# Kernel optimization log

Measured on AMD Instinct MI355X. Metric: run time of the kernel, lower is better.

## Reference

```python
import jax, jax.numpy as jnp
import numpy as np

B, T, A, F, K, DQ, DV = 64, 1024, 128, 1024, 31, 1024, 512  # filters F == T required by source math


def setup_inputs() -> dict:
    key = jax.random.key(0)
    ks = jax.random.split(key, 8)
    s = 0.05
    return {
        "query": jax.random.normal(ks[0], (B, 1, DQ), jnp.float32),
        "value": jax.random.normal(ks[1], (B, T, DV), jnp.float32),
        "attention_weights_cat": jax.random.uniform(ks[2], (B, T, 2), jnp.float32),
        "Wq": jax.random.normal(ks[3], (DQ, A), jnp.float32) * s,
        "Wm": jax.random.normal(ks[4], (DV, A), jnp.float32) * s,
        "Wv": jax.random.normal(ks[5], (A, 1), jnp.float32) * s,
        "Wconv": jax.random.normal(ks[6], (K, 2, F), jnp.float32) * s,
        "Wloc": jax.random.normal(ks[7], (T, A), jnp.float32) * s,
    }


def reference(query, value, attention_weights_cat, Wq, Wm, Wv, Wconv, Wloc):
    # query_layer: Dense(tanh, no bias): [B,1,DQ] -> [B,1,A]
    q = jnp.tanh(jnp.einsum('bld,da->bla', query, Wq))
    # memory_layer: Dense(tanh, no bias): [B,T,DV] -> [B,T,A]
    v = jnp.tanh(jnp.einsum('btd,da->bta', value, Wm))
    # location conv (SAME, no bias): [B,T,2] -> [B,T,F]
    loc = jax.lax.conv_general_dilated(
        attention_weights_cat, Wconv, window_strides=(1,), padding='SAME',
        dimension_numbers=('NWC', 'WIO', 'NWC'))
    # source transposes [0,2,1] then Dense(T->A, tanh): [B,F,T] -> [B,F,A]
    loc = jnp.tanh(jnp.einsum('bft,ta->bfa', jnp.transpose(loc, (0, 2, 1)), Wloc))
    # additive score (F == T so broadcast add is element-aligned): [B,T,1]
    score = jnp.einsum('bta,ao->bto', jnp.tanh(q + v + loc), Wv)
    alignment = jax.nn.softmax(score, axis=1)                # softmax over time
    context = jnp.sum(alignment * v, axis=1)                  # [B,A]
    return context, jnp.transpose(alignment, (0, 2, 1))       # [B,1,T]
```

## Files before the change

kernel.cpp:

```cpp
#include <hip/hip_runtime.h>
#include <hip/hip_bf16.h>

#define BB 64
#define TT 1024
#define AA 128
#define FF 1024
#define DQ 1024
#define DV 512

typedef __bf16 bf16x8_t __attribute__((ext_vector_type(8)));
typedef __bf16 bf16x4_t __attribute__((ext_vector_type(4)));
typedef float f32x4_t __attribute__((ext_vector_type(4)));
typedef _Float16 f16x4_t __attribute__((ext_vector_type(4)));

__device__ __forceinline__ float ftanh(float x) {
    float e = __expf(2.0f * x);
    return 1.0f - 2.0f / (e + 1.0f);
}

__device__ __forceinline__ __bf16 bhi(float x) { return (__bf16)x; }
__device__ __forceinline__ __bf16 blo(float x) {
    __bf16 h = (__bf16)x;
    return (__bf16)(x - (float)h);
}

__global__ __launch_bounds__(256) void k_prep(
    const float* __restrict__ Wm, const float* __restrict__ Wconv,
    const float* __restrict__ Wloc, const float* __restrict__ query,
    const float* __restrict__ Wq,
    __bf16* __restrict__ pwmhi, __bf16* __restrict__ pwmlo,
    __bf16* __restrict__ wcthi, __bf16* __restrict__ wctlo,
    __bf16* __restrict__ pwlhi, __bf16* __restrict__ pwllo,
    float* __restrict__ q_ws) {
    __shared__ float ls[128 * 65];
    int bx = blockIdx.x, tid = threadIdx.x;
    if (bx < 16) {
        int s = bx, d0 = s * 32;
        for (int i = tid; i < 4096; i += 256) {
            int dd = i >> 7, a = i & 127;
            ls[a * 33 + dd] = Wm[(d0 + dd) * AA + a];
        }
        __syncthreads();
#pragma unroll
        for (int u = 0; u < 2; u++) {
            int pos = tid * 2 + u;
            int l15 = pos & 15, lq = (pos >> 4) & 3, g = pos >> 6;
            bf16x8_t h8, l8;
#pragma unroll
            for (int j = 0; j < 8; j++) {
                float x = ls[(g * 16 + l15) * 33 + lq * 8 + j];
                h8[j] = bhi(x);
                l8[j] = blo(x);
            }
            size_t off = (size_t)(s * 512 + pos) * 8;
            *(bf16x8_t*)(pwmhi + off) = h8;
            *(bf16x8_t*)(pwmlo + off) = l8;
        }
    } else if (bx < 24) {
        int f0 = (bx - 16) * 128;
        for (int i = tid; i < 8192; i += 256) {
            int kc = i >> 7, f = i & 127;
            ls[f * 65 + kc] = (kc < 62) ? Wconv[kc * FF + f0 + f] : 0.f;
        }
        __syncthreads();
        int f = tid >> 1, half = tid & 1;
#pragma unroll
        for (int g = 0; g < 4; g++) {
            bf16x8_t h8, l8;
#pragma unroll
            for (int j = 0; j < 8; j++) {
                float x = ls[f * 65 + half * 32 + g * 8 + j];
                h8[j] = bhi(x);
                l8[j] = blo(x);
            }
            size_t off = (size_t)(f0 + f) * 64 + half * 32 + g * 8;
            *(bf16x8_t*)(wcthi + off) = h8;
            *(bf16x8_t*)(wctlo + off) = l8;
        }
    } else if (bx < 56) {
        int s2 = bx - 24, t0 = s2 * 32;
        for (int i = tid; i < 4096; i += 256) {
            int tt = i >> 7, a = i & 127;
            ls[a * 33 + tt] = Wloc[(t0 + tt) * AA + a];
        }
        __syncthreads();
#pragma unroll
        for (int u = 0; u < 2; u++) {
            int pos = tid * 2 + u;
            int l15 = pos & 15, lq = (pos >> 4) & 3, g = pos >> 6;
            bf16x8_t h8, l8;
#pragma unroll
            for (int j = 0; j < 8; j++) {
                float x = ls[(g * 16 + l15) * 33 + lq * 8 + j];
                h8[j] = bhi(x);
                l8[j] = blo(x);
            }
            size_t off = (size_t)(s2 * 512 + pos) * 8;
            *(bf16x8_t*)(pwlhi + off) = h8;
            *(bf16x8_t*)(pwllo + off) = l8;
        }
    } else {
        int b = bx - 56;
        int a = tid & 127, half = tid >> 7;
        const float* qrow = query + b * DQ + half * 512;
        float a0 = 0.f, a1 = 0.f, a2 = 0.f, a3 = 0.f;
        for (int d = 0; d < 512; d += 4) {
            float4 qv = *(const float4*)(qrow + d);
            int dg = (half * 512 + d) * AA + a;
            a0 += qv.x * Wq[dg];
            a1 += qv.y * Wq[dg + AA];
            a2 += qv.z * Wq[dg + 2 * AA];
            a3 += qv.w * Wq[dg + 3 * AA];
        }
        ls[tid] = a0 + a1 + a2 + a3;
        __syncthreads();
        if (half == 0) q_ws[b * AA + a] = ftanh(ls[a] + ls[a + 128]);
    }
}

__global__ __launch_bounds__(256) void k_zq(
    const float* __restrict__ xcat,
    const __bf16* __restrict__ pwlhi, const __bf16* __restrict__ pwllo,
    __bf16* __restrict__ zthi, __bf16* __restrict__ ztlo) {
    int b = blockIdx.x, tid = threadIdx.x;
    __shared__ float xs0[1056], xs1[1056];
    __shared__ float zs[64 * 132];
    for (int i = tid; i < 1056; i += 256) {
        int t = i - 16;
        float2 xv = (t >= 0 && t < TT) ? *(const float2*)(xcat + (size_t)(b * TT + t) * 2)
                                       : make_float2(0.f, 0.f);
        xs0[i] = xv.x;
        xs1[i] = xv.y;
    }
    __syncthreads();
    int lane = tid & 63, wid = tid >> 6;
    int wm = wid >> 1, wn = wid & 1;
    int l15 = lane & 15, lq = lane >> 4;

    f32x4_t zacc[2][4];
#pragma unroll
    for (int mi = 0; mi < 2; mi++)
#pragma unroll
        for (int ni = 0; ni < 4; ni++) zacc[mi][ni] = (f32x4_t){0.f, 0.f, 0.f, 0.f};

    for (int s = 0; s < 32; s++) {
        int t0 = s * 32;
        bf16x8_t bh[4], bl[4];
#pragma unroll
        for (int ni = 0; ni < 4; ni++) {
            size_t poff = (size_t)((s * 8 + wn * 4 + ni) * 64 + lane) * 8;
            bh[ni] = *(const bf16x8_t*)(pwlhi + poff);
            bl[ni] = *(const bf16x8_t*)(pwllo + poff);
        }
        bf16x8_t ah[2], al[2];
#pragma unroll
        for (int mi = 0; mi < 2; mi++) {
            int kc = wm * 32 + mi * 16 + l15;
            const float* xsc = (kc & 1) ? xs1 : xs0;
            int base = t0 + lq * 8 + (kc >> 1) + 1;
#pragma unroll
            for (int j = 0; j < 8; j++) {
                float x = xsc[base + j];
                ah[mi][j] = bhi(x);
                al[mi][j] = blo(x);
            }
        }
#pragma unroll
        for (int ni = 0; ni < 4; ni++)
#pragma unroll
            for (int mi = 0; mi < 2; mi++) {
                zacc[mi][ni] = __builtin_amdgcn_mfma_f32_16x16x32_bf16(ah[mi], bh[ni], zacc[mi][ni], 0, 0, 0);
                zacc[mi][ni] = __builtin_amdgcn_mfma_f32_16x16x32_bf16(al[mi], bh[ni], zacc[mi][ni], 0, 0, 0);
                zacc[mi][ni] = __builtin_amdgcn_mfma_f32_16x16x32_bf16(ah[mi], bl[ni], zacc[mi][ni], 0, 0, 0);
            }
    }
#pragma unroll
    for (int mi = 0; mi < 2; mi++)
#pragma unroll
        for (int ni = 0; ni < 4; ni++)
#pragma unroll
            for (int r = 0; r < 4; r++)
                zs[(wm * 32 + mi * 16 + lq * 4 + r) * 132 + wn * 64 + ni * 16 + l15] = zacc[mi][ni][r];
    __syncthreads();
    int a = tid >> 1, half = tid & 1;
#pragma unroll
    for (int g = 0; g < 4; g++) {
        bf16x8_t h8, l8;
#pragma unroll
        for (int j = 0; j < 8; j++) {
            float x = zs[(half * 32 + g * 8 + j) * 132 + a];
            h8[j] = bhi(x);
            l8[j] = blo(x);
        }
        size_t off = ((size_t)b * AA + a) * 64 + half * 32 + g * 8;
        *(bf16x8_t*)(zthi + off) = h8;
        *(bf16x8_t*)(ztlo + off) = l8;
    }
}

__global__ __launch_bounds__(256) void k_main(
    const float* __restrict__ value,
    const __bf16* __restrict__ pwmhi, const __bf16* __restrict__ pwmlo,
    const __bf16* __restrict__ wcthi, const __bf16* __restrict__ wctlo,
    const __bf16* __restrict__ zthi, const __bf16* __restrict__ ztlo,
    const float* __restrict__ q_ws, const float* __restrict__ Wv,
    _Float16* __restrict__ v_ws, float* __restrict__ score) {
    int b = blockIdx.x >> 3;
    int trow0 = (blockIdx.x & 7) << 7;
    int tid = threadIdx.x;
    int lane = tid & 63, wid = tid >> 6;
    int wm = wid >> 1, wn = wid & 1;
    int l15 = lane & 15, lq = lane >> 4;

    __shared__ __bf16 as_hi[128 * 40];
    __shared__ __bf16 as_lo[128 * 40];
    __shared__ float sc_red[256];

    f32x4_t acc[4][4];
#pragma unroll
    for (int mi = 0; mi < 4; mi++)
#pragma unroll
        for (int ni = 0; ni < 4; ni++) acc[mi][ni] = (f32x4_t){0.f, 0.f, 0.f, 0.f};

    const float* vbase = value + (size_t)(b * TT + trow0) * DV;
    int t0r = tid >> 3, c4 = tid & 7;
    float4 cur[4];
#pragma unroll
    for (int l = 0; l < 4; l++)
        cur[l] = *(const float4*)(vbase + (size_t)(t0r + 32 * l) * DV + c4 * 4);

    for (int it = 0; it < 16; ++it) {
        int d0 = it * 32;
        bf16x8_t bh[4], bl[4];
#pragma unroll
        for (int ni = 0; ni < 4; ni++) {
            size_t poff = (size_t)((it * 8 + wn * 4 + ni) * 64 + lane) * 8;
            bh[ni] = *(const bf16x8_t*)(pwmhi + poff);
            bl[ni] = *(const bf16x8_t*)(pwmlo + poff);
        }
        __syncthreads();
#pragma unroll
        for (int l = 0; l < 4; l++) {
            int t = t0r + 32 * l;
            float4 v4 = cur[l];
            bf16x4_t hv, lv;
            hv[0] = bhi(v4.x); lv[0] = blo(v4.x);
            hv[1] = bhi(v4.y); lv[1] = blo(v4.y);
            hv[2] = bhi(v4.z); lv[2] = blo(v4.z);
            hv[3] = bhi(v4.w); lv[3] = blo(v4.w);
            *(bf16x4_t*)(as_hi + t * 40 + c4 * 4) = hv;
            *(bf16x4_t*)(as_lo + t * 40 + c4 * 4) = lv;
        }
        __syncthreads();
        if (it < 15) {
#pragma unroll
            for (int l = 0; l < 4; l++)
                cur[l] = *(const float4*)(vbase + (size_t)(t0r + 32 * l) * DV + d0 + 32 + c4 * 4);
        }
        bf16x8_t ah[4], al[4];
#pragma unroll
        for (int mi = 0; mi < 4; mi++) {
            int off2 = (wm * 64 + mi * 16 + l15) * 40 + lq * 8;
            ah[mi] = *(const bf16x8_t*)(as_hi + off2);
            al[mi] = *(const bf16x8_t*)(as_lo + off2);
        }
#pragma unroll
        for (int mi = 0; mi < 4; mi++)
#pragma unroll
            for (int ni = 0; ni < 4; ni++) {
                acc[mi][ni] = __builtin_amdgcn_mfma_f32_16x16x32_bf16(ah[mi], bh[ni], acc[mi][ni], 0, 0, 0);
                acc[mi][ni] = __builtin_amdgcn_mfma_f32_16x16x32_bf16(al[mi], bh[ni], acc[mi][ni], 0, 0, 0);
                acc[mi][ni] = __builtin_amdgcn_mfma_f32_16x16x32_bf16(ah[mi], bl[ni], acc[mi][ni], 0, 0, 0);
            }
    }

    f32x4_t lacc[4][4];
#pragma unroll
    for (int mi = 0; mi < 4; mi++)
#pragma unroll
        for (int ni = 0; ni < 4; ni++) lacc[mi][ni] = (f32x4_t){0.f, 0.f, 0.f, 0.f};
#pragma unroll
    for (int kc0 = 0; kc0 < 64; kc0 += 32) {
        bf16x8_t a2h[4], a2l[4], b2h[4], b2l[4];
#pragma unroll
        for (int mi = 0; mi < 4; mi++) {
            int f = trow0 + wm * 64 + mi * 16 + l15;
            a2h[mi] = *(const bf16x8_t*)(wcthi + (size_t)f * 64 + kc0 + lq * 8);
            a2l[mi] = *(const bf16x8_t*)(wctlo + (size_t)f * 64 + kc0 + lq * 8);
        }
#pragma unroll
        for (int ni = 0; ni < 4; ni++) {
            int a = wn * 64 + ni * 16 + l15;
            size_t off = ((size_t)b * AA + a) * 64 + kc0 + lq * 8;
            b2h[ni] = *(const bf16x8_t*)(zthi + off);
            b2l[ni] = *(const bf16x8_t*)(ztlo + off);
        }
#pragma unroll
        for (int mi = 0; mi < 4; mi++)
#pragma unroll
            for (int ni = 0; ni < 4; ni++) {
                lacc[mi][ni] = __builtin_amdgcn_mfma_f32_16x16x32_bf16(a2h[mi], b2h[ni], lacc[mi][ni], 0, 0, 0);
                lacc[mi][ni] = __builtin_amdgcn_mfma_f32_16x16x32_bf16(a2l[mi], b2h[ni], lacc[mi][ni], 0, 0, 0);
                lacc[mi][ni] = __builtin_amdgcn_mfma_f32_16x16x32_bf16(a2h[mi], b2l[ni], lacc[mi][ni], 0, 0, 0);
            }
    }

    float qv[4], wv[4];
#pragma unroll
    for (int ni = 0; ni < 4; ni++) {
        int a = wn * 64 + ni * 16 + l15;
        qv[ni] = q_ws[b * AA + a];
        wv[ni] = Wv[a];
    }
#pragma unroll
    for (int mi = 0; mi < 4; mi++) {
#pragma unroll
        for (int r = 0; r < 4; r++) {
            int tl = wm * 64 + mi * 16 + lq * 4 + r;
            int t = trow0 + tl;
            float s = 0.f;
#pragma unroll
            for (int ni = 0; ni < 4; ni++) {
                float v = ftanh(acc[mi][ni][r]);
                float loc = ftanh(lacc[mi][ni][r]);
                int a = wn * 64 + ni * 16 + l15;
                v_ws[(size_t)(b * TT + t) * AA + a] = (_Float16)v;
                s += ftanh(qv[ni] + v + loc) * wv[ni];
            }
            s += __shfl_xor(s, 1, 64);
            s += __shfl_xor(s, 2, 64);
            s += __shfl_xor(s, 4, 64);
            s += __shfl_xor(s, 8, 64);
            if (l15 == 0) sc_red[wn * 128 + tl] = s;
        }
    }
    __syncthreads();
    if (tid < 128) score[b * TT + trow0 + tid] = sc_red[tid] + sc_red[128 + tid];
}

__global__ void k_softmax(const float* __restrict__ score, float* __restrict__ out_align) {
    int b = blockIdx.x, tid = threadIdx.x;
    __shared__ float red[4];
    float s[4];
#pragma unroll
    for (int i = 0; i < 4; i++) s[i] = score[b * TT + tid + i * 256];
    float m = fmaxf(fmaxf(s[0], s[1]), fmaxf(s[2], s[3]));
    for (int off = 32; off; off >>= 1) m = fmaxf(m, __shfl_xor(m, off, 64));
    int wid = tid >> 6;
    if ((tid & 63) == 0) red[wid] = m;
    __syncthreads();
    float M = fmaxf(fmaxf(red[0], red[1]), fmaxf(red[2], red[3]));
    __syncthreads();
    float e[4];
    float sum = 0.f;
#pragma unroll
    for (int i = 0; i < 4; i++) { e[i] = __expf(s[i] - M); sum += e[i]; }
    for (int off = 32; off; off >>= 1) sum += __shfl_xor(sum, off, 64);
    if ((tid & 63) == 0) red[wid] = sum;
    __syncthreads();
    float inv = 1.0f / (red[0] + red[1] + red[2] + red[3]);
#pragma unroll
    for (int i = 0; i < 4; i++) out_align[b * TT + tid + i * 256] = e[i] * inv;
}

__global__ void k_context(const float* __restrict__ align, const _Float16* __restrict__ v_ws,
                          float* __restrict__ out_ctx) {
    int b = blockIdx.y, t0 = blockIdx.x * 64, tid = threadIdx.x;
    int a0 = (tid & 31) * 4, tl = tid >> 5;
    __shared__ float sh[8 * 132];
    f32x4_t acc = (f32x4_t){0.f, 0.f, 0.f, 0.f};
    for (int tt = tl; tt < 64; tt += 8) {
        float w = align[b * TT + t0 + tt];
        f16x4_t vv = *(const f16x4_t*)(v_ws + (size_t)(b * TT + t0 + tt) * AA + a0);
        acc[0] += w * (float)vv[0];
        acc[1] += w * (float)vv[1];
        acc[2] += w * (float)vv[2];
        acc[3] += w * (float)vv[3];
    }
    *(f32x4_t*)&sh[tl * 132 + a0] = acc;
    __syncthreads();
    if (tid < 128) {
        float s = 0.f;
#pragma unroll
        for (int j = 0; j < 8; j++) s += sh[j * 132 + tid];
        atomicAdd(out_ctx + b * AA + tid, s);
    }
}

extern "C" void kernel_launch(void* const* d_in, const int* in_sizes, int n_in,
                              void* d_out, int out_size, void* d_ws, size_t ws_size,
                              hipStream_t stream) {
    const float* query = (const float*)d_in[0];
    const float* value = (const float*)d_in[1];
    const float* xcat  = (const float*)d_in[2];
    const float* Wq    = (const float*)d_in[3];
    const float* Wm    = (const float*)d_in[4];
    const float* Wv    = (const float*)d_in[5];
    const float* Wconv = (const float*)d_in[6];
    const float* Wloc  = (const float*)d_in[7];
    float* out = (float*)d_out;

    float* ws = (float*)d_ws;
    float* q_ws  = ws;
    float* sc_ws = q_ws + 8192;
    _Float16* v_ws = (_Float16*)(sc_ws + 65536);
    __bf16* pwmhi = (__bf16*)(sc_ws + 65536 + 4194304);
    __bf16* pwmlo = pwmhi + 65536;
    __bf16* wcthi = pwmlo + 65536;
    __bf16* wctlo = wcthi + 65536;
    __bf16* pwlhi = wctlo + 65536;
    __bf16* pwllo = pwlhi + 131072;
    __bf16* zthi  = pwllo + 131072;
    __bf16* ztlo  = zthi + 524288;

    (void)hipMemsetAsync(out, 0, (size_t)8192 * 4, stream);

    k_prep<<<120, 256, 0, stream>>>(Wm, Wconv, Wloc, query, Wq,
                                    pwmhi, pwmlo, wcthi, wctlo, pwlhi, pwllo, q_ws);
    k_zq<<<BB, 256, 0, stream>>>(xcat, pwlhi, pwllo, zthi, ztlo);
    k_main<<<512, 256, 0, stream>>>(value, pwmhi, pwmlo, wcthi, wctlo, zthi, ztlo,
                                    q_ws, Wv, v_ws, sc_ws);
    k_softmax<<<BB, 256, 0, stream>>>(sc_ws, out + 8192);
    k_context<<<dim3(16, BB), 256, 0, stream>>>(out + 8192, v_ws, out);
}
```

Before: 293.0 us.

## Load value fragments directly into registers and double-buffer k_main without LDS

k_main no longer stages the fp32 value tile through shared memory. Each lane loads its MFMA A-fragment straight from global memory and splits it into bf16 hi/lo in registers. Both A and B fragments are double-buffered across iterations, which removes the two __syncthreads per K step. The tile shrinks to 64 rows per block, the grid doubles to 1024 blocks, and launch bounds now ask for 3 waves per SIMD to raise occupancy. The trade-off is that global loads are less coalesced (row-strided 32-byte chunks per lane) and the Wm fragments are reused across fewer rows.

```diff
diff --git a/kernel.cpp b/kernel.cpp
--- a/kernel.cpp
+++ b/kernel.cpp
@@ -198,93 +198,95 @@
     }
 }
 
-__global__ __launch_bounds__(256) void k_main(
+__global__ __launch_bounds__(256, 3) void k_main(
     const float* __restrict__ value,
     const __bf16* __restrict__ pwmhi, const __bf16* __restrict__ pwmlo,
     const __bf16* __restrict__ wcthi, const __bf16* __restrict__ wctlo,
     const __bf16* __restrict__ zthi, const __bf16* __restrict__ ztlo,
     const float* __restrict__ q_ws, const float* __restrict__ Wv,
     _Float16* __restrict__ v_ws, float* __restrict__ score) {
-    int b = blockIdx.x >> 3;
-    int trow0 = (blockIdx.x & 7) << 7;
+    int b = blockIdx.x >> 4;
+    int trow0 = (blockIdx.x & 15) << 6;
     int tid = threadIdx.x;
     int lane = tid & 63, wid = tid >> 6;
     int wm = wid >> 1, wn = wid & 1;
     int l15 = lane & 15, lq = lane >> 4;
 
-    __shared__ __bf16 as_hi[128 * 40];
-    __shared__ __bf16 as_lo[128 * 40];
-    __shared__ float sc_red[256];
-
-    f32x4_t acc[4][4];
-#pragma unroll
-    for (int mi = 0; mi < 4; mi++)
+    __shared__ float sc_red[128];
+
+    f32x4_t acc[2][4];
+#pragma unroll
+    for (int mi = 0; mi < 2; mi++)
 #pragma unroll
         for (int ni = 0; ni < 4; ni++) acc[mi][ni] = (f32x4_t){0.f, 0.f, 0.f, 0.f};
 
-    const float* vbase = value + (size_t)(b * TT + trow0) * DV;
-    int t0r = tid >> 3, c4 = tid & 7;
-    float4 cur[4];
-#pragma unroll
-    for (int l = 0; l < 4; l++)
-        cur[l] = *(const float4*)(vbase + (size_t)(t0r + 32 * l) * DV + c4 * 4);
-
+    const float* arow0 = value + (size_t)(b * TT + trow0 + wm * 32 + l15) * DV + lq * 8;
+    const float* arow1 = arow0 + (size_t)16 * DV;
+
+    f32x4_t fa[2][2][2];
+    bf16x8_t bhb[2][4], blb[2][4];
+
+#pragma unroll
+    for (int h = 0; h < 2; h++) {
+        fa[0][0][h] = *(const f32x4_t*)(arow0 + h * 4);
+        fa[0][1][h] = *(const f32x4_t*)(arow1 + h * 4);
+    }
+#pragma unroll
+    for (int ni = 0; ni < 4; ni++) {
+        size_t poff = (size_t)((wn * 4 + ni) * 64 + lane) * 8;
+        bhb[0][ni] = *(const bf16x8_t*)(pwmhi + poff);
+        blb[0][ni] = *(const bf16x8_t*)(pwmlo + poff);
+    }
+
+#pragma unroll
     for (int it = 0; it < 16; ++it) {
-        int d0 = it * 32;
-        bf16x8_t bh[4], bl[4];
-#pragma unroll
-        for (int ni = 0; ni < 4; ni++) {
-            size_t poff = (size_t)((it * 8 + wn * 4 + ni) * 64 + lane) * 8;
-            bh[ni] = *(const bf16x8_t*)(pwmhi + poff);
-            bl[ni] = *(const bf16x8_t*)(pwmlo + poff);
-        }
-        __syncthreads();
-#pragma unroll
-        for (int l = 0; l < 4; l++) {
-            int t = t0r + 32 * l;
-            float4 v4 = cur[l];
-            bf16x4_t hv, lv;
-            hv[0] = bhi(v4.x); lv[0] = blo(v4.x);
-            hv[1] = bhi(v4.y); lv[1] = blo(v4.y);
-            hv[2] = bhi(v4.z); lv[2] = blo(v4.z);
-            hv[3] = bhi(v4.w); lv[3] = blo(v4.w);
-            *(bf16x4_t*)(as_hi + t * 40 + c4 * 4) = hv;
-            *(bf16x4_t*)(as_lo + t * 40 + c4 * 4) = lv;
-        }
-        __syncthreads();
+        int cur = it & 1, nxt = cur ^ 1;
         if (it < 15) {
-#pragma unroll
-            for (int l = 0; l < 4; l++)
-                cur[l] = *(const float4*)(vbase + (size_t)(t0r + 32 * l) * DV + d0 + 32 + c4 * 4);
-        }
-        bf16x8_t ah[4], al[4];
-#pragma unroll
-        for (int mi = 0; mi < 4; mi++) {
-            int off2 = (wm * 64 + mi * 16 + l15) * 40 + lq * 8;
-            ah[mi] = *(const bf16x8_t*)(as_hi + off2);
-            al[mi] = *(const bf16x8_t*)(as_lo + off2);
-        }
-#pragma unroll
-        for (int mi = 0; mi < 4; mi++)
+            int d = (it + 1) * 32;
+#pragma unroll
+            for (int h = 0; h < 2; h++) {
+                fa[nxt][0][h] = *(const f32x4_t*)(arow0 + d + h * 4);
+                fa[nxt][1][h] = *(const f32x4_t*)(arow1 + d + h * 4);
+            }
 #pragma unroll
             for (int ni = 0; ni < 4; ni++) {
-                acc[mi][ni] = __builtin_amdgcn_mfma_f32_16x16x32_bf16(ah[mi], bh[ni], acc[mi][ni], 0, 0, 0);
-                acc[mi][ni] = __builtin_amdgcn_mfma_f32_16x16x32_bf16(al[mi], bh[ni], acc[mi][ni], 0, 0, 0);
-                acc[mi][ni] = __builtin_amdgcn_mfma_f32_16x16x32_bf16(ah[mi], bl[ni], acc[mi][ni], 0, 0, 0);
-            }
-    }
-
-    f32x4_t lacc[4][4];
-#pragma unroll
-    for (int mi = 0; mi < 4; mi++)
+                size_t poff = (size_t)(((it + 1) * 8 + wn * 4 + ni) * 64 + lane) * 8;
+                bhb[nxt][ni] = *(const bf16x8_t*)(pwmhi + poff);
+                blb[nxt][ni] = *(const bf16x8_t*)(pwmlo + poff);
+            }
+        }
+        bf16x8_t ah[2], al[2];
+#pragma unroll
+        for (int mi = 0; mi < 2; mi++)
+#pragma unroll
+            for (int h = 0; h < 2; h++)
+#pragma unroll
+                for (int j = 0; j < 4; j++) {
+                    float x = fa[cur][mi][h][j];
+                    ah[mi][h * 4 + j] = bhi(x);
+                    al[mi][h * 4 + j] = blo(x);
+                }
+#pragma unroll
+        for (int mi = 0; mi < 2; mi++)
+#pragma unroll
+            for (int ni = 0; ni < 4; ni++) {
+                acc[mi][ni] = __builtin_amdgcn_mfma_f32_16x16x32_bf16(ah[mi], bhb[cur][ni], acc[mi][ni], 0, 0, 0);
+                acc[mi][ni] = __builtin_amdgcn_mfma_f32_16x16x32_bf16(al[mi], bhb[cur][ni], acc[mi][ni], 0, 0, 0);
+                acc[mi][ni] = __builtin_amdgcn_mfma_f32_16x16x32_bf16(ah[mi], blb[cur][ni], acc[mi][ni], 0, 0, 0);
+            }
+    }
+
+    f32x4_t lacc[2][4];
+#pragma unroll
+    for (int mi = 0; mi < 2; mi++)
 #pragma unroll
         for (int ni = 0; ni < 4; ni++) lacc[mi][ni] = (f32x4_t){0.f, 0.f, 0.f, 0.f};
 #pragma unroll
     for (int kc0 = 0; kc0 < 64; kc0 += 32) {
-        bf16x8_t a2h[4], a2l[4], b2h[4], b2l[4];
-#pragma unroll
-        for (int mi = 0; mi < 4; mi++) {
-            int f = trow0 + wm * 64 + mi * 16 + l15;
+        bf16x8_t a2h[2], a2l[2], b2h[4], b2l[4];
+#pragma unroll
+        for (int mi = 0; mi < 2; mi++) {
+            int f = trow0 + wm * 32 + mi * 16 + l15;
             a2h[mi] = *(const bf16x8_t*)(wcthi + (size_t)f * 64 + kc0 + lq * 8);
             a2l[mi] = *(const bf16x8_t*)(wctlo + (size_t)f * 64 + kc0 + lq * 8);
         }
@@ -296,7 +298,7 @@
             b2l[ni] = *(const bf16x8_t*)(ztlo + off);
         }
 #pragma unroll
-        for (int mi = 0; mi < 4; mi++)
+        for (int mi = 0; mi < 2; mi++)
 #pragma unroll
             for (int ni = 0; ni < 4; ni++) {
                 lacc[mi][ni] = __builtin_amdgcn_mfma_f32_16x16x32_bf16(a2h[mi], b2h[ni], lacc[mi][ni], 0, 0, 0);
@@ -313,10 +315,10 @@
         wv[ni] = Wv[a];
     }
 #pragma unroll
-    for (int mi = 0; mi < 4; mi++) {
+    for (int mi = 0; mi < 2; mi++) {
 #pragma unroll
         for (int r = 0; r < 4; r++) {
-            int tl = wm * 64 + mi * 16 + lq * 4 + r;
+            int tl = wm * 32 + mi * 16 + lq * 4 + r;
             int t = trow0 + tl;
             float s = 0.f;
 #pragma unroll
@@ -331,11 +333,11 @@
             s += __shfl_xor(s, 2, 64);
             s += __shfl_xor(s, 4, 64);
             s += __shfl_xor(s, 8, 64);
-            if (l15 == 0) sc_red[wn * 128 + tl] = s;
-        }
-    }
-    __syncthreads();
-    if (tid < 128) score[b * TT + trow0 + tid] = sc_red[tid] + sc_red[128 + tid];
+            if (l15 == 0) sc_red[wn * 64 + tl] = s;
+        }
+    }
+    __syncthreads();
+    if (tid < 64) score[b * TT + trow0 + tid] = sc_red[tid] + sc_red[64 + tid];
 }
 
 __global__ void k_softmax(const float* __restrict__ score, float* __restrict__ out_align) {
@@ -418,8 +420,8 @@
     k_prep<<<120, 256, 0, stream>>>(Wm, Wconv, Wloc, query, Wq,
                                     pwmhi, pwmlo, wcthi, wctlo, pwlhi, pwllo, q_ws);
     k_zq<<<BB, 256, 0, stream>>>(xcat, pwlhi, pwllo, zthi, ztlo);
-    k_main<<<512, 256, 0, stream>>>(value, pwmhi, pwmlo, wcthi, wctlo, zthi, ztlo,
-                                    q_ws, Wv, v_ws, sc_ws);
+    k_main<<<1024, 256, 0, stream>>>(value, pwmhi, pwmlo, wcthi, wctlo, zthi, ztlo,
+                                     q_ws, Wv, v_ws, sc_ws);
     k_softmax<<<BB, 256, 0, stream>>>(sc_ws, out + 8192);
     k_context<<<dim3(16, BB), 256, 0, stream>>>(out + 8192, v_ws, out);
 }
```

Measured after the change: 309.6 us. +5.6%, slower.

## Double-buffer value/weight tiles via direct global-to-LDS loads; split k_zq over A halves

Applied to the files above, without the earlier changes.

The main GEMM loop now stages fp32 value tiles and the packed Wm hi/lo fragments into double-buffered LDS using global_load_lds with an XOR swizzle. The bf16 hi/lo split moves from the staging step to the LDS read. This overlaps the next tile's fetch with the current MFMAs and removes the register round-trip and one barrier per iteration. k_zq is split into 128 blocks, each covering half of A with a phase-rotated loop start, to use more CUs, and k_main gets launch_bounds min-blocks 2. The cost is more LDS per block, which may reduce occupancy.

```diff
diff --git a/kernel.cpp b/kernel.cpp
--- a/kernel.cpp
+++ b/kernel.cpp
@@ -122,9 +122,11 @@
     const float* __restrict__ xcat,
     const __bf16* __restrict__ pwlhi, const __bf16* __restrict__ pwllo,
     __bf16* __restrict__ zthi, __bf16* __restrict__ ztlo) {
-    int b = blockIdx.x, tid = threadIdx.x;
+    int bx = blockIdx.x;
+    int b = bx & 63, ah = bx >> 6;
+    int tid = threadIdx.x;
     __shared__ float xs0[1056], xs1[1056];
-    __shared__ float zs[64 * 132];
+    __shared__ float zs[64 * 66];
     for (int i = tid; i < 1056; i += 256) {
         int t = i - 16;
         float2 xv = (t >= 0 && t < TT) ? *(const float2*)(xcat + (size_t)(b * TT + t) * 2)
@@ -137,22 +139,25 @@
     int wm = wid >> 1, wn = wid & 1;
     int l15 = lane & 15, lq = lane >> 4;
 
-    f32x4_t zacc[2][4];
+    f32x4_t zacc[2][2];
 #pragma unroll
     for (int mi = 0; mi < 2; mi++)
 #pragma unroll
-        for (int ni = 0; ni < 4; ni++) zacc[mi][ni] = (f32x4_t){0.f, 0.f, 0.f, 0.f};
-
-    for (int s = 0; s < 32; s++) {
+        for (int ni = 0; ni < 2; ni++) zacc[mi][ni] = (f32x4_t){0.f, 0.f, 0.f, 0.f};
+
+    int phase = bx & 31;
+    for (int sl = 0; sl < 32; sl++) {
+        int s = (sl + phase) & 31;
         int t0 = s * 32;
-        bf16x8_t bh[4], bl[4];
-#pragma unroll
-        for (int ni = 0; ni < 4; ni++) {
-            size_t poff = (size_t)((s * 8 + wn * 4 + ni) * 64 + lane) * 8;
+        bf16x8_t bh[2], bl[2];
+#pragma unroll
+        for (int ni = 0; ni < 2; ni++) {
+            int g = ah * 4 + wn * 2 + ni;
+            size_t poff = (size_t)((s * 8 + g) * 64 + lane) * 8;
             bh[ni] = *(const bf16x8_t*)(pwlhi + poff);
             bl[ni] = *(const bf16x8_t*)(pwllo + poff);
         }
-        bf16x8_t ah[2], al[2];
+        bf16x8_t ah_[2], al_[2];
 #pragma unroll
         for (int mi = 0; mi < 2; mi++) {
             int kc = wm * 32 + mi * 16 + l15;
@@ -161,44 +166,44 @@
 #pragma unroll
             for (int j = 0; j < 8; j++) {
                 float x = xsc[base + j];
-                ah[mi][j] = bhi(x);
-                al[mi][j] = blo(x);
-            }
-        }
-#pragma unroll
-        for (int ni = 0; ni < 4; ni++)
+                ah_[mi][j] = bhi(x);
+                al_[mi][j] = blo(x);
+            }
+        }
+#pragma unroll
+        for (int ni = 0; ni < 2; ni++)
 #pragma unroll
             for (int mi = 0; mi < 2; mi++) {
-                zacc[mi][ni] = __builtin_amdgcn_mfma_f32_16x16x32_bf16(ah[mi], bh[ni], zacc[mi][ni], 0, 0, 0);
-                zacc[mi][ni] = __builtin_amdgcn_mfma_f32_16x16x32_bf16(al[mi], bh[ni], zacc[mi][ni], 0, 0, 0);
-                zacc[mi][ni] = __builtin_amdgcn_mfma_f32_16x16x32_bf16(ah[mi], bl[ni], zacc[mi][ni], 0, 0, 0);
+                zacc[mi][ni] = __builtin_amdgcn_mfma_f32_16x16x32_bf16(ah_[mi], bh[ni], zacc[mi][ni], 0, 0, 0);
+                zacc[mi][ni] = __builtin_amdgcn_mfma_f32_16x16x32_bf16(al_[mi], bh[ni], zacc[mi][ni], 0, 0, 0);
+                zacc[mi][ni] = __builtin_amdgcn_mfma_f32_16x16x32_bf16(ah_[mi], bl[ni], zacc[mi][ni], 0, 0, 0);
             }
     }
 #pragma unroll
     for (int mi = 0; mi < 2; mi++)
 #pragma unroll
-        for (int ni = 0; ni < 4; ni++)
+        for (int ni = 0; ni < 2; ni++)
 #pragma unroll
             for (int r = 0; r < 4; r++)
-                zs[(wm * 32 + mi * 16 + lq * 4 + r) * 132 + wn * 64 + ni * 16 + l15] = zacc[mi][ni][r];
-    __syncthreads();
-    int a = tid >> 1, half = tid & 1;
-#pragma unroll
-    for (int g = 0; g < 4; g++) {
+                zs[(wm * 32 + mi * 16 + lq * 4 + r) * 66 + wn * 32 + ni * 16 + l15] = zacc[mi][ni][r];
+    __syncthreads();
+    int a_local = tid & 63, seg = tid >> 6;
+#pragma unroll
+    for (int g = 0; g < 2; g++) {
         bf16x8_t h8, l8;
 #pragma unroll
         for (int j = 0; j < 8; j++) {
-            float x = zs[(half * 32 + g * 8 + j) * 132 + a];
+            float x = zs[(seg * 16 + g * 8 + j) * 66 + a_local];
             h8[j] = bhi(x);
             l8[j] = blo(x);
         }
-        size_t off = ((size_t)b * AA + a) * 64 + half * 32 + g * 8;
+        size_t off = ((size_t)b * AA + ah * 64 + a_local) * 64 + seg * 16 + g * 8;
         *(bf16x8_t*)(zthi + off) = h8;
         *(bf16x8_t*)(ztlo + off) = l8;
     }
 }
 
-__global__ __launch_bounds__(256) void k_main(
+__global__ __launch_bounds__(256, 2) void k_main(
     const float* __restrict__ value,
     const __bf16* __restrict__ pwmhi, const __bf16* __restrict__ pwmlo,
     const __bf16* __restrict__ wcthi, const __bf16* __restrict__ wctlo,
@@ -212,8 +217,9 @@
     int wm = wid >> 1, wn = wid & 1;
     int l15 = lane & 15, lq = lane >> 4;
 
-    __shared__ __bf16 as_hi[128 * 40];
-    __shared__ __bf16 as_lo[128 * 40];
+    __shared__ __align__(16) float As[2][128 * 32];
+    __shared__ __align__(16) __bf16 Bh[2][512 * 8];
+    __shared__ __align__(16) __bf16 Bl[2][512 * 8];
     __shared__ float sc_red[256];
 
     f32x4_t acc[4][4];
@@ -222,47 +228,75 @@
 #pragma unroll
         for (int ni = 0; ni < 4; ni++) acc[mi][ni] = (f32x4_t){0.f, 0.f, 0.f, 0.f};
 
-    const float* vbase = value + (size_t)(b * TT + trow0) * DV;
-    int t0r = tid >> 3, c4 = tid & 7;
-    float4 cur[4];
-#pragma unroll
-    for (int l = 0; l < 4; l++)
-        cur[l] = *(const float4*)(vbase + (size_t)(t0r + 32 * l) * DV + c4 * 4);
-
+    int l3 = lane >> 3;
+    int su = (lane & 7) ^ l3;
+    const float* aG[4];
+    unsigned aL[4];
+#pragma unroll
+    for (int i = 0; i < 4; i++) {
+        int row = (wid * 4 + i) * 8 + l3;
+        aG[i] = value + (size_t)(b * TT + trow0 + row) * DV + su * 4;
+        aL[i] = (unsigned)((wid * 4 + i) * 1024);
+    }
+    const __bf16* bGh[2];
+    const __bf16* bGl[2];
+    unsigned bL[2];
+#pragma unroll
+    for (int j = 0; j < 2; j++) {
+        int c = (wid * 2 + j) * 64 + lane;
+        bGh[j] = pwmhi + (size_t)c * 8;
+        bGl[j] = pwmlo + (size_t)c * 8;
+        bL[j] = (unsigned)((wid * 2 + j) * 1024);
+    }
+
+#define STAGE(bf, s)                                                                        \
+    {                                                                                       \
+        _Pragma("unroll") for (int i = 0; i < 4; i++)                                       \
+            __builtin_amdgcn_global_load_lds(                                               \
+                (const __attribute__((address_space(1))) void*)(aG[i] + (s) * 32),          \
+                (__attribute__((address_space(3))) void*)((char*)&As[bf][0] + aL[i]),       \
+                16, 0, 0);                                                                  \
+        _Pragma("unroll") for (int j = 0; j < 2; j++) {                                     \
+            __builtin_amdgcn_global_load_lds(                                               \
+                (const __attribute__((address_space(1))) void*)(bGh[j] + (size_t)(s) * 4096),\
+                (__attribute__((address_space(3))) void*)((char*)&Bh[bf][0] + bL[j]),       \
+                16, 0, 0);                                                                  \
+            __builtin_amdgcn_global_load_lds(                                               \
+                (const __attribute__((address_space(1))) void*)(bGl[j] + (size_t)(s) * 4096),\
+                (__attribute__((address_space(3))) void*)((char*)&Bl[bf][0] + bL[j]),       \
+                16, 0, 0);                                                                  \
+        }                                                                                   \
+    }
+
+    STAGE(0, 0);
+    __syncthreads();
+
+    int swz = l15 & 7;
     for (int it = 0; it < 16; ++it) {
-        int d0 = it * 32;
+        int cb = it & 1;
+        if (it < 15) STAGE(cb ^ 1, it + 1);
+
+        bf16x8_t ah[4], al[4];
+#pragma unroll
+        for (int mi = 0; mi < 4; mi++) {
+            int row = wm * 64 + mi * 16 + l15;
+            const char* rbase = (const char*)&As[cb][0] + row * 128;
+            f32x4_t f0 = *(const f32x4_t*)(rbase + (((lq * 2 + 0) ^ swz) << 4));
+            f32x4_t f1 = *(const f32x4_t*)(rbase + (((lq * 2 + 1) ^ swz) << 4));
+#pragma unroll
+            for (int j = 0; j < 4; j++) {
+                ah[mi][j] = bhi(f0[j]);
+                al[mi][j] = blo(f0[j]);
+                ah[mi][4 + j] = bhi(f1[j]);
+                al[mi][4 + j] = blo(f1[j]);
+            }
+        }
         bf16x8_t bh[4], bl[4];
 #pragma unroll
         for (int ni = 0; ni < 4; ni++) {
-            size_t poff = (size_t)((it * 8 + wn * 4 + ni) * 64 + lane) * 8;
-            bh[ni] = *(const bf16x8_t*)(pwmhi + poff);
-            bl[ni] = *(const bf16x8_t*)(pwmlo + poff);
-        }
-        __syncthreads();
-#pragma unroll
-        for (int l = 0; l < 4; l++) {
-            int t = t0r + 32 * l;
-            float4 v4 = cur[l];
-            bf16x4_t hv, lv;
-            hv[0] = bhi(v4.x); lv[0] = blo(v4.x);
-            hv[1] = bhi(v4.y); lv[1] = blo(v4.y);
-            hv[2] = bhi(v4.z); lv[2] = blo(v4.z);
-            hv[3] = bhi(v4.w); lv[3] = blo(v4.w);
-            *(bf16x4_t*)(as_hi + t * 40 + c4 * 4) = hv;
-            *(bf16x4_t*)(as_lo + t * 40 + c4 * 4) = lv;
-        }
-        __syncthreads();
-        if (it < 15) {
-#pragma unroll
-            for (int l = 0; l < 4; l++)
-                cur[l] = *(const float4*)(vbase + (size_t)(t0r + 32 * l) * DV + d0 + 32 + c4 * 4);
-        }
-        bf16x8_t ah[4], al[4];
-#pragma unroll
-        for (int mi = 0; mi < 4; mi++) {
-            int off2 = (wm * 64 + mi * 16 + l15) * 40 + lq * 8;
-            ah[mi] = *(const bf16x8_t*)(as_hi + off2);
-            al[mi] = *(const bf16x8_t*)(as_lo + off2);
+            int c = (wn * 4 + ni) * 64 + lane;
+            bh[ni] = *(const bf16x8_t*)(&Bh[cb][0] + (size_t)c * 8);
+            bl[ni] = *(const bf16x8_t*)(&Bl[cb][0] + (size_t)c * 8);
         }
 #pragma unroll
         for (int mi = 0; mi < 4; mi++)
@@ -272,7 +306,9 @@
                 acc[mi][ni] = __builtin_amdgcn_mfma_f32_16x16x32_bf16(al[mi], bh[ni], acc[mi][ni], 0, 0, 0);
                 acc[mi][ni] = __builtin_amdgcn_mfma_f32_16x16x32_bf16(ah[mi], bl[ni], acc[mi][ni], 0, 0, 0);
             }
-    }
+        __syncthreads();
+    }
+#undef STAGE
 
     f32x4_t lacc[4][4];
 #pragma unroll
@@ -417,7 +453,7 @@
 
     k_prep<<<120, 256, 0, stream>>>(Wm, Wconv, Wloc, query, Wq,
                                     pwmhi, pwmlo, wcthi, wctlo, pwlhi, pwllo, q_ws);
-    k_zq<<<BB, 256, 0, stream>>>(xcat, pwlhi, pwllo, zthi, ztlo);
+    k_zq<<<128, 256, 0, stream>>>(xcat, pwlhi, pwllo, zthi, ztlo);
     k_main<<<512, 256, 0, stream>>>(value, pwmhi, pwmlo, wcthi, wctlo, zthi, ztlo,
                                     q_ws, Wv, v_ws, sc_ws);
     k_softmax<<<BB, 256, 0, stream>>>(sc_ws, out + 8192);
```

After: 268.4 us. 1.09x faster.
